# Performance work log

Measured on AMD Instinct MI355X. Metric: run time of the kernel, lower is better.

Reference implementation:

```python
import jax, jax.numpy as jnp
import numpy as np

HIDDEN = 1024
HEADS = 16
HEAD_DIM = HIDDEN // HEADS


def setup_inputs() -> dict:
    key = jax.random.key(0)
    ks = jax.random.split(key, 4)
    B, S, H = 2, 2048, HIDDEN
    scale = 1.0 / np.sqrt(H)
    return {
        "inputs": jax.random.normal(ks[0], (B, S, H), dtype=jnp.float32),
        "mask": jnp.ones((B, S), dtype=jnp.int32),
        "Wq": jax.random.normal(ks[1], (H, H), dtype=jnp.float32) * scale,
        "bq": jnp.zeros((H,), dtype=jnp.float32),
        "Wk": jax.random.normal(ks[2], (H, H), dtype=jnp.float32) * scale,
        "bk": jnp.zeros((H,), dtype=jnp.float32),
        "Wv": jax.random.normal(ks[3], (H, H), dtype=jnp.float32) * scale,
        "bv": jnp.zeros((H,), dtype=jnp.float32),
    }


def _split_heads(x, B, S):
    # [B,S,H] -> [B,heads,S,head_dim]
    return x.reshape(B, S, HEADS, HEAD_DIM).transpose(0, 2, 1, 3)


def reference(inputs, mask, Wq, bq, Wk, bk, Wv, bv):
    B, S, H = inputs.shape
    q = _split_heads(inputs @ Wq.T + bq, B, S)
    k = _split_heads(inputs @ Wk.T + bk, B, S)
    v = _split_heads(inputs @ Wv.T + bv, B, S)
    scores = jnp.einsum("bhqd,bhkd->bhqk", q, k) / jnp.sqrt(
        jnp.asarray(HEAD_DIM, dtype=inputs.dtype))
    # mask broadcast [B,1,1,S]; zeros -> -inf
    scores = jnp.where(mask[:, None, None, :] == 0, -jnp.inf, scores)
    attn = jax.nn.softmax(scores, axis=-1)
    context = jnp.einsum("bhqk,bhkd->bhqd", attn, v)
    return context.transpose(0, 2, 1, 3).reshape(B, S, H)
```

## Files before the change

kernel.cpp:

```cpp
#include <hip/hip_runtime.h>
#include <hip/hip_fp16.h>

constexpr int S_LEN  = 2048;
constexpr int HID    = 1024;
constexpr int HEADS  = 16;
constexpr int HDIM   = 64;
constexpr int BATCH  = 2;
constexpr int BH     = BATCH * HEADS;
constexpr int M_ROWS = BATCH * S_LEN;

typedef _Float16 half8  __attribute__((ext_vector_type(8)));
typedef _Float16 half4v __attribute__((ext_vector_type(4)));
typedef _Float16 half2v __attribute__((ext_vector_type(2)));
typedef float    f32x4  __attribute__((ext_vector_type(4)));
typedef float    f32x16 __attribute__((ext_vector_type(16)));

constexpr float EXP2_OFF = -11.541560327111707f;
constexpr float Q_SCALE  = 0.18033688011112042f;

__global__ __launch_bounds__(256) void cvt_kernel(
    const float* __restrict__ X,  const float* __restrict__ Wq,
    const float* __restrict__ Wk, const float* __restrict__ Wv,
    const int* __restrict__ mask,
    _Float16* __restrict__ Xh,  _Float16* __restrict__ Wqh,
    _Float16* __restrict__ Wkh, _Float16* __restrict__ Wvh,
    float* __restrict__ maskF)
{
    const int blk = blockIdx.x;
    if (blk >= 3584) {
        const int loc = blk - 3584;
        const size_t e = ((size_t)loc * 256 + threadIdx.x) * 8;
        #pragma unroll
        for (int i = 0; i < 8; ++i)
            maskF[e + i] = mask[e + i] ? EXP2_OFF : -1.0e30f;
        return;
    }
    const float* src; _Float16* dst; int loc;
    if (blk < 2048)      { src = X;  dst = Xh;  loc = blk; }
    else if (blk < 2560) { src = Wq; dst = Wqh; loc = blk - 2048; }
    else if (blk < 3072) { src = Wk; dst = Wkh; loc = blk - 2560; }
    else                 { src = Wv; dst = Wvh; loc = blk - 3072; }
    const size_t e = ((size_t)loc * 256 + threadIdx.x) * 8;
    float4 a = *reinterpret_cast<const float4*>(&src[e]);
    float4 b = *reinterpret_cast<const float4*>(&src[e + 4]);
    half8 h = { (_Float16)a.x, (_Float16)a.y, (_Float16)a.z, (_Float16)a.w,
                (_Float16)b.x, (_Float16)b.y, (_Float16)b.z, (_Float16)b.w };
    *reinterpret_cast<half8*>(&dst[e]) = h;
}

__device__ __forceinline__ void async_cp16(_Float16* lds, const _Float16* g) {
    __builtin_amdgcn_global_load_lds(
        (const __attribute__((address_space(1))) void*)g,
        (__attribute__((address_space(3))) void*)lds, 16, 0, 0);
}

__global__ __launch_bounds__(256) void qkv_proj_kernel(
    const _Float16* __restrict__ Xh,
    const _Float16* __restrict__ Wqh, const _Float16* __restrict__ Wkh,
    const _Float16* __restrict__ Wvh,
    const float* __restrict__ bq, const float* __restrict__ bk,
    const float* __restrict__ bv,
    _Float16* __restrict__ Qo, _Float16* __restrict__ Ko,
    _Float16* __restrict__ Vt)
{
    const int mode = blockIdx.z;
    const _Float16* W    = (mode == 0) ? Wqh : (mode == 1) ? Wkh : Wvh;
    const float*    bias = (mode == 0) ? bq  : (mode == 1) ? bk  : bv;

    const int m0 = blockIdx.x * 128, n0 = blockIdx.y * 128;
    const int tid = threadIdx.x, wave = tid >> 6, lane = tid & 63;
    const int l31 = lane & 31, kg = lane >> 5;

    __shared__ _Float16 SMEM[18432];

    f32x16 acc[2][2];
    #pragma unroll
    for (int mt = 0; mt < 2; ++mt)
        #pragma unroll
        for (int nt = 0; nt < 2; ++nt)
            #pragma unroll
            for (int i = 0; i < 16; ++i) acc[mt][nt][i] = 0.f;

    const int wm = (wave & 1) * 64, wn = (wave >> 1) * 64;

    const int srow = tid >> 2, spos = tid & 3;
    auto stage = [&](int k0, int b) {
        _Float16* Asb = SMEM + b * 8192;
        _Float16* Bsb = Asb + 4096;
        #pragma unroll
        for (int j = 0; j < 2; ++j) {
            const int row = srow + j * 64;
            const int sch = spos ^ (row & 3);
            async_cp16(&Asb[j * 2048 + tid * 8],
                       &Xh[(size_t)(m0 + row) * HID + k0 + sch * 8]);
            async_cp16(&Bsb[j * 2048 + tid * 8],
                       &W [(size_t)(n0 + row) * HID + k0 + sch * 8]);
        }
    };

    stage(0, 0);
    int buf = 0;

    for (int k0 = 0; k0 < HID; k0 += 32) {
        __syncthreads();
        if (k0 + 32 < HID) stage(k0 + 32, buf ^ 1);
        _Float16* Asb = SMEM + buf * 8192;
        _Float16* Bsb = Asb + 4096;

        #pragma unroll
        for (int c = 0; c < 2; ++c) {
            const int k8 = c * 2 + kg;
            half8 af[2], bf[2];
            #pragma unroll
            for (int mt = 0; mt < 2; ++mt) {
                const int row = wm + mt * 32 + l31;
                af[mt] = *reinterpret_cast<const half8*>(
                    &Asb[row * 32 + ((k8 ^ (row & 3)) * 8)]);
            }
            #pragma unroll
            for (int nt = 0; nt < 2; ++nt) {
                const int row = wn + nt * 32 + l31;
                bf[nt] = *reinterpret_cast<const half8*>(
                    &Bsb[row * 32 + ((k8 ^ (row & 3)) * 8)]);
            }
            #pragma unroll
            for (int mt = 0; mt < 2; ++mt)
                #pragma unroll
                for (int nt = 0; nt < 2; ++nt)
                    acc[mt][nt] = __builtin_amdgcn_mfma_f32_32x32x16_f16(
                        af[mt], bf[nt], acc[mt][nt], 0, 0, 0);
        }
        buf ^= 1;
    }
    __syncthreads();

    _Float16* T = SMEM + wave * 4608;

    const int nn  = n0 + wn;
    const int hh  = nn >> 6;
    const int mm  = m0 + wm;
    const int bb  = mm >> 11;
    const int bhv = bb * HEADS + hh;
    const int s0  = mm & 2047;
    const int rowg = lane >> 3, chunk = lane & 7;

    if (mode < 2) {
        _Float16* Out = (mode == 0) ? Qo : Ko;
        #pragma unroll
        for (int nt = 0; nt < 2; ++nt) {
            const int col = nt * 32 + l31;
            float bias_n = bias[nn + col];
            #pragma unroll
            for (int mt = 0; mt < 2; ++mt)
                #pragma unroll
                for (int r = 0; r < 16; ++r) {
                    const int row_l = (r & 3) + 8 * (r >> 2) + 4 * kg;
                    float v = acc[mt][nt][r] + bias_n;
                    if (mode == 0) v *= Q_SCALE;
                    T[(mt * 32 + row_l) * 72 + col] = (_Float16)v;
                }
        }
        asm volatile("s_waitcnt lgkmcnt(0)" ::: "memory");
        #pragma unroll
        for (int j = 0; j < 8; ++j) {
            const int sr = j * 8 + rowg;
            half8 v = *reinterpret_cast<const half8*>(&T[sr * 72 + chunk * 8]);
            *reinterpret_cast<half8*>(
                &Out[((size_t)bhv * S_LEN + s0 + sr) * HDIM + chunk * 8]) = v;
        }
    } else {
        #pragma unroll
        for (int nt = 0; nt < 2; ++nt) {
            const int col = nt * 32 + l31;
            const float bias_n = bias[nn + col];
            #pragma unroll
            for (int mt = 0; mt < 2; ++mt)
                #pragma unroll
                for (int rg = 0; rg < 4; ++rg) {
                    half4v t = { (_Float16)(acc[mt][nt][rg * 4 + 0] + bias_n),
                                 (_Float16)(acc[mt][nt][rg * 4 + 1] + bias_n),
                                 (_Float16)(acc[mt][nt][rg * 4 + 2] + bias_n),
                                 (_Float16)(acc[mt][nt][rg * 4 + 3] + bias_n) };
                    const int s_off = mt * 32 + 8 * rg + 4 * kg;
                    *reinterpret_cast<half4v*>(&T[col * 72 + s_off]) = t;
                }
        }
        asm volatile("s_waitcnt lgkmcnt(0)" ::: "memory");
        #pragma unroll
        for (int j = 0; j < 8; ++j) {
            const int dr = j * 8 + rowg;
            half8 v = *reinterpret_cast<const half8*>(&T[dr * 72 + chunk * 8]);
            *reinterpret_cast<half8*>(
                &Vt[((size_t)bhv * HDIM + dr) * S_LEN + s0 + chunk * 8]) = v;
        }
    }
}

__global__ __launch_bounds__(256) void attn_kernel(
    const _Float16* __restrict__ Q, const _Float16* __restrict__ K,
    const _Float16* __restrict__ Vt, const float* __restrict__ maskF,
    float* __restrict__ Out)
{
    const int id    = blockIdx.x;
    const int xcd   = id & 7, local = id >> 3;
    const int bh    = xcd * 4 + (local & 3);
    const int qt    = local >> 2;
    const int b = bh >> 4, h = bh & 15;
    const int tid = threadIdx.x, wave = tid >> 6, lane = tid & 63;
    const int l15 = lane & 15, quad = lane >> 4;

    __shared__ _Float16 Ks[2][64 * 64];
    __shared__ _Float16 Vs[2][64 * 64];
    __shared__ _Float16 Ps[4][32][68];

    const _Float16* Qb = Q  + (size_t)bh * S_LEN * HDIM;
    const _Float16* Kb = K  + (size_t)bh * S_LEN * HDIM;
    const _Float16* Vb = Vt + (size_t)bh * HDIM * S_LEN;
    const float*    mb = maskF + b * S_LEN;

    const int qrow0 = qt * 128 + wave * 32 + l15;
    half8 qf[2][2];
    #pragma unroll
    for (int g = 0; g < 2; ++g) {
        const size_t qo = (size_t)(qrow0 + g * 16) * HDIM;
        qf[g][0] = *reinterpret_cast<const half8*>(&Qb[qo + quad * 8]);
        qf[g][1] = *reinterpret_cast<const half8*>(&Qb[qo + 32 + quad * 8]);
    }

    f32x4 acc[2][4];
    #pragma unroll
    for (int g = 0; g < 2; ++g)
        #pragma unroll
        for (int mt = 0; mt < 4; ++mt) acc[g][mt] = (f32x4){0.f, 0.f, 0.f, 0.f};
    float den[2] = {0.f, 0.f};

    const int srow_t = tid >> 3;
    const int sch    = (tid & 7) ^ (srow_t & 7);
    auto stage = [&](int kb, int buf) {
        #pragma unroll
        for (int j = 0; j < 2; ++j) {
            const int row = srow_t + j * 32;
            async_cp16(&Ks[buf][j * 2048 + tid * 8],
                       &Kb[(size_t)(kb + row) * HDIM + sch * 8]);
            async_cp16(&Vs[buf][j * 2048 + tid * 8],
                       &Vb[(size_t)row * S_LEN + kb + sch * 8]);
        }
    };

    stage(0, 0);
    int buf = 0;
    const int rsw = (l15 & 7);

    for (int kb = 0; kb < S_LEN; kb += 64) {
        __syncthreads();
        if (kb + 64 < S_LEN) stage(kb + 64, buf ^ 1);

        float4 m4[4];
        #pragma unroll
        for (int nt = 0; nt < 4; ++nt)
            m4[nt] = *reinterpret_cast<const float4*>(&mb[kb + nt * 16 + quad * 4]);

        half8 kf[2][4];
        #pragma unroll
        for (int c = 0; c < 2; ++c)
            #pragma unroll
            for (int nt = 0; nt < 4; ++nt)
                kf[c][nt] = *reinterpret_cast<const half8*>(
                    &Ks[buf][(nt * 16 + l15) * 64 + ((c * 4 + quad) ^ rsw) * 8]);
        half8 vf[2][4];
        #pragma unroll
        for (int c = 0; c < 2; ++c)
            #pragma unroll
            for (int mt = 0; mt < 4; ++mt)
                vf[c][mt] = *reinterpret_cast<const half8*>(
                    &Vs[buf][(mt * 16 + l15) * 64 + ((c * 4 + quad) ^ rsw) * 8]);

        #pragma unroll
        for (int g = 0; g < 2; ++g) {
            f32x4 sc[4];
            #pragma unroll
            for (int nt = 0; nt < 4; ++nt) sc[nt] = (f32x4){0.f, 0.f, 0.f, 0.f};
            #pragma unroll
            for (int c = 0; c < 2; ++c)
                #pragma unroll
                for (int nt = 0; nt < 4; ++nt)
                    sc[nt] = __builtin_amdgcn_mfma_f32_16x16x32_f16(
                        kf[c][nt], qf[g][c], sc[nt], 0, 0, 0);

            #pragma unroll
            for (int nt = 0; nt < 4; ++nt) {
                float p0 = __builtin_amdgcn_exp2f(sc[nt][0] + m4[nt].x);
                float p1 = __builtin_amdgcn_exp2f(sc[nt][1] + m4[nt].y);
                float p2 = __builtin_amdgcn_exp2f(sc[nt][2] + m4[nt].z);
                float p3 = __builtin_amdgcn_exp2f(sc[nt][3] + m4[nt].w);
                den[g] += (p0 + p1) + (p2 + p3);
                half2v lo = __builtin_bit_cast(half2v, __builtin_amdgcn_cvt_pkrtz(p0, p1));
                half2v hi = __builtin_bit_cast(half2v, __builtin_amdgcn_cvt_pkrtz(p2, p3));
                half4v pk = { lo[0], lo[1], hi[0], hi[1] };
                *reinterpret_cast<half4v*>(
                    &Ps[wave][g * 16 + l15][nt * 16 + quad * 4]) = pk;
            }
        }
        asm volatile("s_waitcnt lgkmcnt(0)" ::: "memory");

        #pragma unroll
        for (int g = 0; g < 2; ++g) {
            #pragma unroll
            for (int c = 0; c < 2; ++c) {
                half4v plo = *reinterpret_cast<const half4v*>(
                    &Ps[wave][g * 16 + l15][c * 32 + quad * 8]);
                half4v phi = *reinterpret_cast<const half4v*>(
                    &Ps[wave][g * 16 + l15][c * 32 + quad * 8 + 4]);
                half8 pf = { plo[0], plo[1], plo[2], plo[3],
                             phi[0], phi[1], phi[2], phi[3] };
                #pragma unroll
                for (int mt = 0; mt < 4; ++mt)
                    acc[g][mt] = __builtin_amdgcn_mfma_f32_16x16x32_f16(
                        vf[c][mt], pf, acc[g][mt], 0, 0, 0);
            }
        }
        buf ^= 1;
    }

    #pragma unroll
    for (int g = 0; g < 2; ++g) {
        float d = den[g];
        d += __shfl_xor(d, 16, 64);
        d += __shfl_xor(d, 32, 64);
        const float inv = 1.0f / d;
        float* orow = Out + ((size_t)(b * S_LEN + qrow0 + g * 16)) * HID + h * HDIM;
        #pragma unroll
        for (int mt = 0; mt < 4; ++mt) {
            float4 o = { acc[g][mt][0] * inv, acc[g][mt][1] * inv,
                         acc[g][mt][2] * inv, acc[g][mt][3] * inv };
            *reinterpret_cast<float4*>(&orow[mt * 16 + quad * 4]) = o;
        }
    }
}

extern "C" void kernel_launch(void* const* d_in, const int* in_sizes, int n_in,
                              void* d_out, int out_size, void* d_ws, size_t ws_size,
                              hipStream_t stream) {
    const float* X  = (const float*)d_in[0];
    const int*   mk = (const int*)  d_in[1];
    const float* Wq = (const float*)d_in[2];
    const float* bq = (const float*)d_in[3];
    const float* Wk = (const float*)d_in[4];
    const float* bk = (const float*)d_in[5];
    const float* Wv = (const float*)d_in[6];
    const float* bv = (const float*)d_in[7];
    float* out = (float*)d_out;

    _Float16* Xh  = (_Float16*)d_ws;
    _Float16* Wqh = Xh  + (size_t)M_ROWS * HID;
    _Float16* Wkh = Wqh + (size_t)HID * HID;
    _Float16* Wvh = Wkh + (size_t)HID * HID;
    _Float16* Q   = Wvh + (size_t)HID * HID;
    _Float16* K   = Q   + (size_t)BH * S_LEN * HDIM;
    _Float16* Vt  = K   + (size_t)BH * S_LEN * HDIM;
    float*    maskF = (float*)(Vt + (size_t)BH * S_LEN * HDIM);

    cvt_kernel<<<3586, 256, 0, stream>>>(X, Wq, Wk, Wv, mk, Xh, Wqh, Wkh, Wvh, maskF);

    dim3 gp(M_ROWS / 128, HID / 128, 3);
    qkv_proj_kernel<<<gp, 256, 0, stream>>>(Xh, Wqh, Wkh, Wvh, bq, bk, bv, Q, K, Vt);

    attn_kernel<<<512, 256, 0, stream>>>(Q, K, Vt, maskF, out);
}
```

Before: 175.1 us.

## Switch attention to 32x32x16 MFMA and pass P through registers via permlane32_swap

Rewrites the attention inner loop to use 32x32x16 MFMA tiles instead of 16x16x32. It feeds the softmax probabilities straight into the PV MFMA by repacking the fp16 values across lane halves with v_permlane32_swap. This removes the per-wave LDS scratch buffer for P, the LDS write/read round-trip and the lgkmcnt wait. The risk is higher register pressure from the 16-wide accumulators, and correctness depends on the permlane layout matching the B-operand format.

```diff
diff --git a/kernel.cpp b/kernel.cpp
--- a/kernel.cpp
+++ b/kernel.cpp
@@ -14,6 +14,7 @@
 typedef _Float16 half2v __attribute__((ext_vector_type(2)));
 typedef float    f32x4  __attribute__((ext_vector_type(4)));
 typedef float    f32x16 __attribute__((ext_vector_type(16)));
+typedef unsigned uint4v __attribute__((ext_vector_type(4)));
 
 constexpr float EXP2_OFF = -11.541560327111707f;
 constexpr float Q_SCALE  = 0.18033688011112042f;
@@ -54,6 +55,10 @@
         (__attribute__((address_space(3))) void*)lds, 16, 0, 0);
 }
 
+__device__ __forceinline__ void permlane32_swap(unsigned &x, unsigned &y) {
+    asm("v_permlane32_swap_b32 %0, %1" : "+v"(x), "+v"(y));
+}
+
 __global__ __launch_bounds__(256) void qkv_proj_kernel(
     const _Float16* __restrict__ Xh,
     const _Float16* __restrict__ Wqh, const _Float16* __restrict__ Wkh,
@@ -207,32 +212,30 @@
     const int qt    = local >> 2;
     const int b = bh >> 4, h = bh & 15;
     const int tid = threadIdx.x, wave = tid >> 6, lane = tid & 63;
-    const int l15 = lane & 15, quad = lane >> 4;
+    const int l31 = lane & 31, kg = lane >> 5;
 
     __shared__ _Float16 Ks[2][64 * 64];
     __shared__ _Float16 Vs[2][64 * 64];
-    __shared__ _Float16 Ps[4][32][68];
 
     const _Float16* Qb = Q  + (size_t)bh * S_LEN * HDIM;
     const _Float16* Kb = K  + (size_t)bh * S_LEN * HDIM;
     const _Float16* Vb = Vt + (size_t)bh * HDIM * S_LEN;
     const float*    mb = maskF + b * S_LEN;
 
-    const int qrow0 = qt * 128 + wave * 32 + l15;
-    half8 qf[2][2];
+    const int qrow = qt * 128 + wave * 32 + l31;
+
+    half8 qf[4];
     #pragma unroll
-    for (int g = 0; g < 2; ++g) {
-        const size_t qo = (size_t)(qrow0 + g * 16) * HDIM;
-        qf[g][0] = *reinterpret_cast<const half8*>(&Qb[qo + quad * 8]);
-        qf[g][1] = *reinterpret_cast<const half8*>(&Qb[qo + 32 + quad * 8]);
-    }
-
-    f32x4 acc[2][4];
+    for (int kc = 0; kc < 4; ++kc)
+        qf[kc] = *reinterpret_cast<const half8*>(
+            &Qb[(size_t)qrow * HDIM + kc * 16 + kg * 8]);
+
+    f32x16 acc[2];
     #pragma unroll
-    for (int g = 0; g < 2; ++g)
-        #pragma unroll
-        for (int mt = 0; mt < 4; ++mt) acc[g][mt] = (f32x4){0.f, 0.f, 0.f, 0.f};
-    float den[2] = {0.f, 0.f};
+    for (int dt = 0; dt < 2; ++dt)
+        #pragma unroll
+        for (int i = 0; i < 16; ++i) acc[dt][i] = 0.f;
+    float den = 0.f;
 
     const int srow_t = tid >> 3;
     const int sch    = (tid & 7) ^ (srow_t & 7);
@@ -249,93 +252,91 @@
 
     stage(0, 0);
     int buf = 0;
-    const int rsw = (l15 & 7);
+    const int rsw = l31 & 7;
 
     for (int kb = 0; kb < S_LEN; kb += 64) {
         __syncthreads();
         if (kb + 64 < S_LEN) stage(kb + 64, buf ^ 1);
 
-        float4 m4[4];
-        #pragma unroll
-        for (int nt = 0; nt < 4; ++nt)
-            m4[nt] = *reinterpret_cast<const float4*>(&mb[kb + nt * 16 + quad * 4]);
-
-        half8 kf[2][4];
-        #pragma unroll
-        for (int c = 0; c < 2; ++c)
-            #pragma unroll
-            for (int nt = 0; nt < 4; ++nt)
-                kf[c][nt] = *reinterpret_cast<const half8*>(
-                    &Ks[buf][(nt * 16 + l15) * 64 + ((c * 4 + quad) ^ rsw) * 8]);
+        f32x16 sc[2];
+        #pragma unroll
+        for (int kt = 0; kt < 2; ++kt) {
+            #pragma unroll
+            for (int i = 0; i < 16; ++i) sc[kt][i] = 0.f;
+            half8 kf[4];
+            #pragma unroll
+            for (int kc = 0; kc < 4; ++kc)
+                kf[kc] = *reinterpret_cast<const half8*>(
+                    &Ks[buf][(kt * 32 + l31) * 64 + (((kc * 2 + kg) ^ rsw) * 8)]);
+            #pragma unroll
+            for (int kc = 0; kc < 4; ++kc)
+                sc[kt] = __builtin_amdgcn_mfma_f32_32x32x16_f16(
+                    kf[kc], qf[kc], sc[kt], 0, 0, 0);
+        }
+
         half8 vf[2][4];
         #pragma unroll
-        for (int c = 0; c < 2; ++c)
-            #pragma unroll
-            for (int mt = 0; mt < 4; ++mt)
-                vf[c][mt] = *reinterpret_cast<const half8*>(
-                    &Vs[buf][(mt * 16 + l15) * 64 + ((c * 4 + quad) ^ rsw) * 8]);
-
-        #pragma unroll
-        for (int g = 0; g < 2; ++g) {
-            f32x4 sc[4];
-            #pragma unroll
-            for (int nt = 0; nt < 4; ++nt) sc[nt] = (f32x4){0.f, 0.f, 0.f, 0.f};
-            #pragma unroll
-            for (int c = 0; c < 2; ++c)
-                #pragma unroll
-                for (int nt = 0; nt < 4; ++nt)
-                    sc[nt] = __builtin_amdgcn_mfma_f32_16x16x32_f16(
-                        kf[c][nt], qf[g][c], sc[nt], 0, 0, 0);
-
-            #pragma unroll
-            for (int nt = 0; nt < 4; ++nt) {
-                float p0 = __builtin_amdgcn_exp2f(sc[nt][0] + m4[nt].x);
-                float p1 = __builtin_amdgcn_exp2f(sc[nt][1] + m4[nt].y);
-                float p2 = __builtin_amdgcn_exp2f(sc[nt][2] + m4[nt].z);
-                float p3 = __builtin_amdgcn_exp2f(sc[nt][3] + m4[nt].w);
-                den[g] += (p0 + p1) + (p2 + p3);
-                half2v lo = __builtin_bit_cast(half2v, __builtin_amdgcn_cvt_pkrtz(p0, p1));
-                half2v hi = __builtin_bit_cast(half2v, __builtin_amdgcn_cvt_pkrtz(p2, p3));
-                half4v pk = { lo[0], lo[1], hi[0], hi[1] };
-                *reinterpret_cast<half4v*>(
-                    &Ps[wave][g * 16 + l15][nt * 16 + quad * 4]) = pk;
+        for (int dt = 0; dt < 2; ++dt)
+            #pragma unroll
+            for (int kc = 0; kc < 4; ++kc)
+                vf[dt][kc] = *reinterpret_cast<const half8*>(
+                    &Vs[buf][(dt * 32 + l31) * 64 + (((kc * 2 + kg) ^ rsw) * 8)]);
+
+        #pragma unroll
+        for (int kt = 0; kt < 2; ++kt) {
+            float4 mm[4];
+            #pragma unroll
+            for (int g = 0; g < 4; ++g)
+                mm[g] = *reinterpret_cast<const float4*>(
+                    &mb[kb + kt * 32 + g * 8 + kg * 4]);
+
+            float p[16];
+            #pragma unroll
+            for (int r = 0; r < 16; ++r) {
+                const float* m4 = reinterpret_cast<const float*>(&mm[r >> 2]);
+                p[r] = __builtin_amdgcn_exp2f(sc[kt][r] + m4[r & 3]);
             }
-        }
-        asm volatile("s_waitcnt lgkmcnt(0)" ::: "memory");
-
-        #pragma unroll
-        for (int g = 0; g < 2; ++g) {
-            #pragma unroll
-            for (int c = 0; c < 2; ++c) {
-                half4v plo = *reinterpret_cast<const half4v*>(
-                    &Ps[wave][g * 16 + l15][c * 32 + quad * 8]);
-                half4v phi = *reinterpret_cast<const half4v*>(
-                    &Ps[wave][g * 16 + l15][c * 32 + quad * 8 + 4]);
-                half8 pf = { plo[0], plo[1], plo[2], plo[3],
-                             phi[0], phi[1], phi[2], phi[3] };
-                #pragma unroll
-                for (int mt = 0; mt < 4; ++mt)
-                    acc[g][mt] = __builtin_amdgcn_mfma_f32_16x16x32_f16(
-                        vf[c][mt], pf, acc[g][mt], 0, 0, 0);
+            den += (((p[0] + p[1]) + (p[2] + p[3])) +
+                    ((p[4] + p[5]) + (p[6] + p[7]))) +
+                   (((p[8] + p[9]) + (p[10] + p[11])) +
+                    ((p[12] + p[13]) + (p[14] + p[15])));
+
+            #pragma unroll
+            for (int hh = 0; hh < 2; ++hh) {
+                unsigned a0 = __builtin_bit_cast(unsigned,
+                    __builtin_amdgcn_cvt_pkrtz(p[hh * 8 + 0], p[hh * 8 + 1]));
+                unsigned a1 = __builtin_bit_cast(unsigned,
+                    __builtin_amdgcn_cvt_pkrtz(p[hh * 8 + 2], p[hh * 8 + 3]));
+                unsigned b0 = __builtin_bit_cast(unsigned,
+                    __builtin_amdgcn_cvt_pkrtz(p[hh * 8 + 4], p[hh * 8 + 5]));
+                unsigned b1 = __builtin_bit_cast(unsigned,
+                    __builtin_amdgcn_cvt_pkrtz(p[hh * 8 + 6], p[hh * 8 + 7]));
+                permlane32_swap(a0, b0);
+                permlane32_swap(a1, b1);
+                uint4v pd = { a0, a1, b0, b1 };
+                half8 pf = __builtin_bit_cast(half8, pd);
+                const int kc2 = kt * 2 + hh;
+                acc[0] = __builtin_amdgcn_mfma_f32_32x32x16_f16(
+                    vf[0][kc2], pf, acc[0], 0, 0, 0);
+                acc[1] = __builtin_amdgcn_mfma_f32_32x32x16_f16(
+                    vf[1][kc2], pf, acc[1], 0, 0, 0);
             }
         }
         buf ^= 1;
     }
 
+    den += __shfl_xor(den, 32, 64);
+    const float inv = 1.0f / den;
+
+    float* orow = Out + ((size_t)(b * S_LEN + qrow)) * HID + h * HDIM;
     #pragma unroll
-    for (int g = 0; g < 2; ++g) {
-        float d = den[g];
-        d += __shfl_xor(d, 16, 64);
-        d += __shfl_xor(d, 32, 64);
-        const float inv = 1.0f / d;
-        float* orow = Out + ((size_t)(b * S_LEN + qrow0 + g * 16)) * HID + h * HDIM;
-        #pragma unroll
-        for (int mt = 0; mt < 4; ++mt) {
-            float4 o = { acc[g][mt][0] * inv, acc[g][mt][1] * inv,
-                         acc[g][mt][2] * inv, acc[g][mt][3] * inv };
-            *reinterpret_cast<float4*>(&orow[mt * 16 + quad * 4]) = o;
-        }
-    }
+    for (int dt = 0; dt < 2; ++dt)
+        #pragma unroll
+        for (int g = 0; g < 4; ++g) {
+            float4 o = { acc[dt][g * 4 + 0] * inv, acc[dt][g * 4 + 1] * inv,
+                         acc[dt][g * 4 + 2] * inv, acc[dt][g * 4 + 3] * inv };
+            *reinterpret_cast<float4*>(&orow[dt * 32 + g * 8 + kg * 4]) = o;
+        }
 }
 
 extern "C" void kernel_launch(void* const* d_in, const int* in_sizes, int n_in,
```

New measurement: 181.6 us. 3.7% more time.
